# Performance work log

Measured on AMD Instinct MI355X. Metric: run time of the kernel, lower is better.

## Reference

```python
import jax, jax.numpy as jnp
import numpy as np


def setup_inputs() -> dict:
    key = jax.random.key(0)
    ks = jax.random.split(key, 6)
    B, T, H, L, V = 8, 100, 1024, 512, 32000
    x = jax.random.normal(ks[0], (B, T, H), dtype=jnp.float32)
    attn_dist = jax.random.normal(ks[1], (B, T, L), dtype=jnp.float32)
    enc_input = jax.random.randint(ks[2], (B, L), 0, V, dtype=jnp.int32)
    W_vocab = jax.random.normal(ks[3], (H, V), dtype=jnp.float32) * (1.0 / np.sqrt(H))
    b_vocab = jnp.zeros((V,), dtype=jnp.float32)
    w_gen = jax.random.normal(ks[4], (H, 1), dtype=jnp.float32) * (1.0 / np.sqrt(H))
    b_gen = jnp.zeros((1,), dtype=jnp.float32)
    return {"x": x, "attn_dist": attn_dist, "enc_input": enc_input,
            "W_vocab": W_vocab, "b_vocab": b_vocab, "w_gen": w_gen, "b_gen": b_gen}


def reference(x, attn_dist, enc_input, W_vocab, b_vocab, w_gen, b_gen):
    B, T, H = x.shape
    L = attn_dist.shape[-1]
    V = W_vocab.shape[-1]
    # generation gate: sigmoid(x @ w_gen + b_gen) -> [B, T, 1]
    p_gen = jax.nn.sigmoid(jnp.einsum('bth,ho->bto', x, w_gen) + b_gen)
    # vocab distribution: softmax over vocab of the projection -> [B, T, V]
    vocab_dist = jax.nn.softmax(jnp.einsum('bth,hv->btv', x, W_vocab) + b_vocab, axis=-1)
    vocab_dist = p_gen * vocab_dist
    # copy distribution over encoder positions -> [B, T, L]
    copy_dist = (1.0 - p_gen) * jax.nn.softmax(attn_dist, axis=-1)
    # scatter-add copy probabilities into vocab slots (duplicates accumulate)
    vd = vocab_dist.reshape(B * T, V)
    cd = copy_dist.reshape(B * T, L)
    idx = jnp.broadcast_to(enc_input[:, None, :], (B, T, L)).reshape(B * T, L)
    rows = jnp.arange(B * T, dtype=jnp.int32)[:, None]
    combined = vd.at[rows, idx].add(cd)
    return jnp.log(combined).reshape(B, T, V)
```

## Files before the change

kernel.cpp:

```cpp
#include <hip/hip_runtime.h>
#include <math.h>

#define BB 8
#define TT 100
#define HH 1024
#define LL 512
#define VV 32000
#define NROWS (BB*TT)
#define MPAD 896
#define NMT 7
#define NNT 250
#define NWG (NMT*NNT)

typedef __bf16 bf16x8 __attribute__((ext_vector_type(8)));
typedef __bf16 bf16x4 __attribute__((ext_vector_type(4)));
typedef float f32x4 __attribute__((ext_vector_type(4)));

__device__ __forceinline__ void gload16(const void* g, void* l) {
  __builtin_amdgcn_global_load_lds(
      (const __attribute__((address_space(1))) unsigned int*)g,
      (__attribute__((address_space(3))) unsigned int*)l, 16, 0, 0);
}

__global__ __launch_bounds__(256) void k_cvt_x(const float* __restrict__ x,
                                               __bf16* __restrict__ xb) {
  int idx = blockIdx.x * 256 + threadIdx.x;
  int row = (idx * 4) >> 10;
  bf16x4 v;
  if (row < NROWS) {
    float4 f = ((const float4*)x)[idx];
    v[0] = (__bf16)f.x; v[1] = (__bf16)f.y; v[2] = (__bf16)f.z; v[3] = (__bf16)f.w;
  } else {
    v[0] = v[1] = v[2] = v[3] = (__bf16)0.f;
  }
  ((bf16x4*)xb)[idx] = v;
}

__global__ __launch_bounds__(256) void k_pgen_copy(
    const float* __restrict__ x, const float* __restrict__ attn,
    const float* __restrict__ w_gen, const float* __restrict__ b_gen,
    float* __restrict__ p_gen, float* __restrict__ copy_dist,
    float* __restrict__ rsum) {
  int r = blockIdx.x;
  int tid = threadIdx.x;
  __shared__ float red[4];
  if (tid == 0) rsum[r] = 0.f;

  float d = 0.f;
  for (int h = tid; h < HH; h += 256) d += x[(size_t)r * HH + h] * w_gen[h];
#pragma unroll
  for (int o = 32; o > 0; o >>= 1) d += __shfl_down(d, o, 64);
  if ((tid & 63) == 0) red[tid >> 6] = d;
  __syncthreads();
  float dot = red[0] + red[1] + red[2] + red[3];
  float p = 1.f / (1.f + __expf(-(dot + b_gen[0])));
  if (tid == 0) p_gen[r] = p;

  float a0 = attn[(size_t)r * LL + tid];
  float a1 = attn[(size_t)r * LL + 256 + tid];
  float m = fmaxf(a0, a1);
#pragma unroll
  for (int o = 32; o > 0; o >>= 1) m = fmaxf(m, __shfl_down(m, o, 64));
  __syncthreads();
  if ((tid & 63) == 0) red[tid >> 6] = m;
  __syncthreads();
  float M = fmaxf(fmaxf(red[0], red[1]), fmaxf(red[2], red[3]));
  float e0 = __expf(a0 - M), e1 = __expf(a1 - M);
  float s = e0 + e1;
#pragma unroll
  for (int o = 32; o > 0; o >>= 1) s += __shfl_down(s, o, 64);
  __syncthreads();
  if ((tid & 63) == 0) red[tid >> 6] = s;
  __syncthreads();
  float S = red[0] + red[1] + red[2] + red[3];
  float scale = (1.f - p) / S;
  copy_dist[(size_t)r * LL + tid] = e0 * scale;
  copy_dist[(size_t)r * LL + 256 + tid] = e1 * scale;
}

__global__ __launch_bounds__(256) void k_gemm_mfma(
    const __bf16* __restrict__ Xb, const float* __restrict__ Wv,
    const float* __restrict__ bias, float* __restrict__ out,
    float* __restrict__ rsum) {
  __shared__ __align__(16) __bf16 As[2][128 * 32];
  __shared__ __align__(16) __bf16 Bs[2][128 * 32];
  int tid = threadIdx.x;
  int lane = tid & 63, wave = tid >> 6;
  int wr = wave >> 1, wc = wave & 1;
  int l15 = lane & 15, quad = lane >> 4;

  int lid = blockIdx.x;
  int xcd = lid & 7, sub = lid >> 3;
  const int q = NWG >> 3, rr = NWG & 7;
  int wg = (xcd < rr) ? (xcd * (q + 1) + sub)
                      : (rr * (q + 1) + (xcd - rr) * q + sub);
  int m0 = (wg % NMT) * 128;
  int n0 = (wg / NMT) * 128;

  f32x4 acc[4][4];
#pragma unroll
  for (int mi = 0; mi < 4; ++mi)
#pragma unroll
    for (int ni = 0; ni < 4; ++ni) acc[mi][ni] = (f32x4){0.f, 0.f, 0.f, 0.f};

  int r0 = wave * 32;
  int lr = lane >> 2;
  int chunk = (lane & 3) ^ ((lr >> 1) & 3);
  const __bf16* aptr0 = Xb + (size_t)(m0 + r0 + lr) * HH + chunk * 8;
  const __bf16* aptr1 = aptr0 + (size_t)16 * HH;
  __bf16* lA0[2] = {&As[0][r0 * 32], &As[1][r0 * 32]};
  __bf16* lA1[2] = {&As[0][(r0 + 16) * 32], &As[1][(r0 + 16) * 32]};

  int nq = tid & 31;
  int kb = tid >> 5;
  const int rn0 = nq * 4;
  const int bslot = (kb >> 1);
  const int bsub = (kb & 1) * 4;
  const float4* wsrc = (const float4*)Wv + (size_t)(kb * 4) * (VV / 4) + (n0 + nq * 4) / 4;

  int sw8 = (quad ^ ((l15 >> 1) & 3)) * 8;

#define STAGEA(it, buf) do {                        \
    gload16(aptr0 + (size_t)(it) * 32, lA0[buf]);   \
    gload16(aptr1 + (size_t)(it) * 32, lA1[buf]);   \
  } while (0)

#define LOADB(it) do {                                          \
    _Pragma("unroll")                                           \
    for (int jj = 0; jj < 4; ++jj)                              \
      wv[jj] = wsrc[(size_t)((it) * 32 + jj) * (VV / 4)];       \
  } while (0)

#define WRITEB(buf) do {                                              \
    _Pragma("unroll")                                                 \
    for (int i = 0; i < 4; ++i) {                                     \
      int rn = rn0 + i;                                               \
      bf16x4 bv;                                                      \
      bv[0] = (__bf16)wv[0][i]; bv[1] = (__bf16)wv[1][i];             \
      bv[2] = (__bf16)wv[2][i]; bv[3] = (__bf16)wv[3][i];             \
      int slot = bslot ^ ((rn >> 1) & 3);                             \
      *(bf16x4*)&Bs[buf][rn * 32 + slot * 8 + bsub] = bv;             \
    }                                                                 \
  } while (0)

#define COMPUTE(buf) do {                                                     \
    const __bf16* Ab = As[buf];                                               \
    const __bf16* Bb = Bs[buf];                                               \
    bf16x8 af[4], bfg[4];                                                     \
    _Pragma("unroll")                                                         \
    for (int mi = 0; mi < 4; ++mi)                                            \
      af[mi] = *(const bf16x8*)&Ab[(wr * 64 + mi * 16 + l15) * 32 + sw8];     \
    _Pragma("unroll")                                                         \
    for (int ni = 0; ni < 4; ++ni)                                            \
      bfg[ni] = *(const bf16x8*)&Bb[(wc * 64 + ni * 16 + l15) * 32 + sw8];    \
    _Pragma("unroll")                                                         \
    for (int mi = 0; mi < 4; ++mi)                                            \
      _Pragma("unroll")                                                       \
      for (int ni = 0; ni < 4; ++ni)                                          \
        acc[mi][ni] = __builtin_amdgcn_mfma_f32_16x16x32_bf16(                \
            af[mi], bfg[ni], acc[mi][ni], 0, 0, 0);                           \
  } while (0)

  float4 wv[4];
  STAGEA(0, 0);
  LOADB(0);
  WRITEB(0);

  for (int it = 0; it < 32; ++it) {
    int cur = it & 1;
    __syncthreads();
    int nxt = cur ^ 1;
    if (it + 1 < 32) {
      STAGEA(it + 1, nxt);
      LOADB(it + 1);
    }
    COMPUTE(cur);
    if (it + 1 < 32) WRITEB(nxt);
  }

  float bv4[4];
#pragma unroll
  for (int ni = 0; ni < 4; ++ni) bv4[ni] = bias[n0 + wc * 64 + ni * 16 + l15];

#pragma unroll
  for (int mi = 0; mi < 4; ++mi) {
#pragma unroll
    for (int rg = 0; rg < 4; ++rg) {
      int row = m0 + wr * 64 + mi * 16 + quad * 4 + rg;
      bool valid = row < NROWS;
      float esum = 0.f;
#pragma unroll
      for (int ni = 0; ni < 4; ++ni) {
        int col = n0 + wc * 64 + ni * 16 + l15;
        float v = acc[mi][ni][rg] + bv4[ni];
        if (valid) out[(size_t)row * VV + col] = v;
        esum += __expf(v);
      }
#pragma unroll
      for (int o = 8; o > 0; o >>= 1) esum += __shfl_down(esum, o, 16);
      if (l15 == 0 && valid) atomicAdd(&rsum[row], esum);
    }
  }
#undef STAGEA
#undef LOADB
#undef WRITEB
#undef COMPUTE
}

__global__ __launch_bounds__(256) void k_affine_scatter(
    float* __restrict__ out, const float* __restrict__ p_gen,
    const float* __restrict__ rsum, const int* __restrict__ enc,
    const float* __restrict__ copy) {
  __shared__ int hkey[1024];
  __shared__ float hval[1024];
  int r = blockIdx.x, tid = threadIdx.x;
  float* row = out + (size_t)r * VV;
  float logc = __logf(p_gen[r] / rsum[r]);
  for (int i = tid; i < 1024; i += 256) { hkey[i] = -1; hval[i] = 0.f; }
  __syncthreads();
  int b = r / TT;
  for (int j = tid; j < LL; j += 256) {
    int v = enc[(size_t)b * LL + j];
    float cv = copy[(size_t)r * LL + j];
    unsigned h = ((unsigned)v * 2654435761u) & 1023u;
    while (true) {
      int prev = atomicCAS(&hkey[h], -1, v);
      if (prev == -1 || prev == v) { atomicAdd(&hval[h], cv); break; }
      h = (h + 1) & 1023u;
    }
  }
  for (int c4 = tid; c4 < VV / 4; c4 += 256) {
    float4 v = ((float4*)row)[c4];
    v.x += logc; v.y += logc; v.z += logc; v.w += logc;
    ((float4*)row)[c4] = v;
  }
  __syncthreads();
  for (int h = tid; h < 1024; h += 256) {
    int col = hkey[h];
    if (col >= 0) {
      float stored = row[col];
      row[col] = __logf(__expf(stored) + hval[h]);
    }
  }
}

extern "C" void kernel_launch(void* const* d_in, const int* in_sizes, int n_in,
                              void* d_out, int out_size, void* d_ws, size_t ws_size,
                              hipStream_t stream) {
  const float* x    = (const float*)d_in[0];
  const float* attn = (const float*)d_in[1];
  const int*   enc  = (const int*)d_in[2];
  const float* Wv   = (const float*)d_in[3];
  const float* bv   = (const float*)d_in[4];
  const float* wgen = (const float*)d_in[5];
  const float* bg   = (const float*)d_in[6];
  float* out = (float*)d_out;
  float* ws = (float*)d_ws;

  float* p_gen = ws;
  float* rsum  = ws + 1024;
  float* copy  = ws + 2048;
  __bf16* xb = (__bf16*)(ws + 2048 + NROWS * LL);

  k_cvt_x<<<MPAD * HH / 4 / 256, 256, 0, stream>>>(x, xb);
  k_pgen_copy<<<NROWS, 256, 0, stream>>>(x, attn, wgen, bg, p_gen, copy, rsum);
  k_gemm_mfma<<<NWG, 256, 0, stream>>>(xb, Wv, bv, out, rsum);
  k_affine_scatter<<<NROWS, 256, 0, stream>>>(out, p_gen, rsum, enc, copy);
}
```

Baseline: 386.9 us.

## Fuse x bf16 conversion into pgen kernel and retune B-tile LDS swizzle

Removes the separate x-to-bf16 conversion kernel and does the conversion inside the p_gen/copy kernel, which already reads x. The launch grows to MPAD blocks so the extra blocks zero the padded rows. This saves one launch and a second read of x. The B-tile LDS swizzle is changed to a different XOR pattern (on nq for writes, l15>>2 for reads) to reduce bank conflicts, and the B global loads are issued before the A async loads.

```diff
diff --git a/kernel.cpp b/kernel.cpp
--- a/kernel.cpp
+++ b/kernel.cpp
@@ -22,32 +22,28 @@
       (__attribute__((address_space(3))) unsigned int*)l, 16, 0, 0);
 }
 
-__global__ __launch_bounds__(256) void k_cvt_x(const float* __restrict__ x,
-                                               __bf16* __restrict__ xb) {
-  int idx = blockIdx.x * 256 + threadIdx.x;
-  int row = (idx * 4) >> 10;
-  bf16x4 v;
-  if (row < NROWS) {
-    float4 f = ((const float4*)x)[idx];
-    v[0] = (__bf16)f.x; v[1] = (__bf16)f.y; v[2] = (__bf16)f.z; v[3] = (__bf16)f.w;
-  } else {
-    v[0] = v[1] = v[2] = v[3] = (__bf16)0.f;
-  }
-  ((bf16x4*)xb)[idx] = v;
-}
-
 __global__ __launch_bounds__(256) void k_pgen_copy(
     const float* __restrict__ x, const float* __restrict__ attn,
     const float* __restrict__ w_gen, const float* __restrict__ b_gen,
     float* __restrict__ p_gen, float* __restrict__ copy_dist,
-    float* __restrict__ rsum) {
+    float* __restrict__ rsum, __bf16* __restrict__ xb) {
   int r = blockIdx.x;
   int tid = threadIdx.x;
+  if (r >= NROWS) {
+    bf16x4 z; z[0] = z[1] = z[2] = z[3] = (__bf16)0.f;
+    ((bf16x4*)(xb + (size_t)r * HH))[tid] = z;
+    return;
+  }
   __shared__ float red[4];
   if (tid == 0) rsum[r] = 0.f;
 
-  float d = 0.f;
-  for (int h = tid; h < HH; h += 256) d += x[(size_t)r * HH + h] * w_gen[h];
+  float4 f = ((const float4*)(x + (size_t)r * HH))[tid];
+  bf16x4 v;
+  v[0] = (__bf16)f.x; v[1] = (__bf16)f.y; v[2] = (__bf16)f.z; v[3] = (__bf16)f.w;
+  ((bf16x4*)(xb + (size_t)r * HH))[tid] = v;
+
+  float4 w = ((const float4*)w_gen)[tid];
+  float d = f.x * w.x + f.y * w.y + f.z * w.z + f.w * w.w;
 #pragma unroll
   for (int o = 32; o > 0; o >>= 1) d += __shfl_down(d, o, 64);
   if ((tid & 63) == 0) red[tid >> 6] = d;
@@ -114,11 +110,13 @@
   int nq = tid & 31;
   int kb = tid >> 5;
   const int rn0 = nq * 4;
-  const int bslot = (kb >> 1);
+  const int bslot = kb >> 1;
   const int bsub = (kb & 1) * 4;
+  const int wslot = bslot ^ (nq & 3);
   const float4* wsrc = (const float4*)Wv + (size_t)(kb * 4) * (VV / 4) + (n0 + nq * 4) / 4;
 
-  int sw8 = (quad ^ ((l15 >> 1) & 3)) * 8;
+  int swA8 = (quad ^ ((l15 >> 1) & 3)) * 8;
+  int swB8 = (quad ^ ((l15 >> 2) & 3)) * 8;
 
 #define STAGEA(it, buf) do {                        \
     gload16(aptr0 + (size_t)(it) * 32, lA0[buf]);   \
@@ -138,8 +136,7 @@
       bf16x4 bv;                                                      \
       bv[0] = (__bf16)wv[0][i]; bv[1] = (__bf16)wv[1][i];             \
       bv[2] = (__bf16)wv[2][i]; bv[3] = (__bf16)wv[3][i];             \
-      int slot = bslot ^ ((rn >> 1) & 3);                             \
-      *(bf16x4*)&Bs[buf][rn * 32 + slot * 8 + bsub] = bv;             \
+      *(bf16x4*)&Bs[buf][rn * 32 + wslot * 8 + bsub] = bv;            \
     }                                                                 \
   } while (0)
 
@@ -149,10 +146,10 @@
     bf16x8 af[4], bfg[4];                                                     \
     _Pragma("unroll")                                                         \
     for (int mi = 0; mi < 4; ++mi)                                            \
-      af[mi] = *(const bf16x8*)&Ab[(wr * 64 + mi * 16 + l15) * 32 + sw8];     \
+      af[mi] = *(const bf16x8*)&Ab[(wr * 64 + mi * 16 + l15) * 32 + swA8];    \
     _Pragma("unroll")                                                         \
     for (int ni = 0; ni < 4; ++ni)                                            \
-      bfg[ni] = *(const bf16x8*)&Bb[(wc * 64 + ni * 16 + l15) * 32 + sw8];    \
+      bfg[ni] = *(const bf16x8*)&Bb[(wc * 64 + ni * 16 + l15) * 32 + swB8];   \
     _Pragma("unroll")                                                         \
     for (int mi = 0; mi < 4; ++mi)                                            \
       _Pragma("unroll")                                                       \
@@ -162,8 +159,8 @@
   } while (0)
 
   float4 wv[4];
+  LOADB(0);
   STAGEA(0, 0);
-  LOADB(0);
   WRITEB(0);
 
   for (int it = 0; it < 32; ++it) {
@@ -171,8 +168,8 @@
     __syncthreads();
     int nxt = cur ^ 1;
     if (it + 1 < 32) {
+      LOADB(it + 1);
       STAGEA(it + 1, nxt);
-      LOADB(it + 1);
     }
     COMPUTE(cur);
     if (it + 1 < 32) WRITEB(nxt);
@@ -262,8 +259,7 @@
   float* copy  = ws + 2048;
   __bf16* xb = (__bf16*)(ws + 2048 + NROWS * LL);
 
-  k_cvt_x<<<MPAD * HH / 4 / 256, 256, 0, stream>>>(x, xb);
-  k_pgen_copy<<<NROWS, 256, 0, stream>>>(x, attn, wgen, bg, p_gen, copy, rsum);
+  k_pgen_copy<<<MPAD, 256, 0, stream>>>(x, attn, wgen, bg, p_gen, copy, rsum, xb);
   k_gemm_mfma<<<NWG, 256, 0, stream>>>(xb, Wv, bv, out, rsum);
   k_affine_scatter<<<NROWS, 256, 0, stream>>>(out, p_gen, rsum, enc, copy);
 }
```

Result: faster. 371.9 us (-3.9%).
